# Optimization experiments

Hardware: AMD Instinct MI355X
Metric: run time of the kernel (lower is better)

Reference implementation:

```python
import jax, jax.numpy as jnp
import numpy as np

B, S, D = 2, 2048, 2048
H, KVH, DH = 16, 4, 128
WIN = 128
THETA = 10000.0  # local rope (layer_idx=0 -> local/sliding path)


def setup_inputs() -> dict:
    key = jax.random.key(0)
    ks = jax.random.split(key, 5)
    return {
        "x": jax.random.normal(ks[0], (B, S, D), dtype=jnp.float32),
        "Wq": jax.random.normal(ks[1], (H * DH, D), dtype=jnp.float32) * 0.02,
        "Wk": jax.random.normal(ks[2], (KVH * DH, D), dtype=jnp.float32) * 0.02,
        "Wv": jax.random.normal(ks[3], (KVH * DH, D), dtype=jnp.float32) * 0.02,
        "Wo": jax.random.normal(ks[4], (D, H * DH), dtype=jnp.float32) * 0.02,
    }


def _rotate_half(t):
    half = t.shape[-1] // 2
    return jnp.concatenate([-t[..., half:], t[..., :half]], axis=-1)


def _rope_tables(seq_len, head_dim, theta, dtype):
    inv_freq = 1.0 / (theta ** (jnp.arange(0, head_dim, 2, dtype=jnp.float32) / head_dim))
    freqs = jnp.arange(seq_len, dtype=jnp.float32)[:, None] * inv_freq[None, :]  # [S, DH/2]
    # source does repeat_interleave(cos, 2, dim=-1): [S, DH]
    cos = jnp.repeat(jnp.cos(freqs), 2, axis=-1).astype(dtype)
    sin = jnp.repeat(jnp.sin(freqs), 2, axis=-1).astype(dtype)
    return cos[None, :, None, :], sin[None, :, None, :]  # broadcast over [B,S,H,DH]


def reference(x, Wq, Wk, Wv, Wo):
    b, s, _ = x.shape
    q = (x @ Wq.T).reshape(b, s, H, DH)
    k = (x @ Wk.T).reshape(b, s, KVH, DH)
    v = (x @ Wv.T).reshape(b, s, KVH, DH)

    cos, sin = _rope_tables(s, DH, THETA, x.dtype)
    q = q * cos + _rotate_half(q) * sin
    k = k * cos + _rotate_half(k) * sin

    # GQA: repeat_interleave kv heads to n_heads
    groups = H // KVH
    k = jnp.repeat(k, groups, axis=2)
    v = jnp.repeat(v, groups, axis=2)

    q = q.transpose(0, 2, 1, 3)  # [B,H,S,DH]
    k = k.transpose(0, 2, 1, 3)
    v = v.transpose(0, 2, 1, 3)

    scale = DH ** -0.5
    scores = jnp.einsum('bhqd,bhkd->bhqk', q, k) * scale  # [B,H,S,S]

    # faithful local mask from source: q_idx >= k_idx - window_size
    iq = jnp.arange(s)[:, None]
    ik = jnp.arange(s)[None, :]
    mask = iq >= (ik - WIN)  # [S,S]
    scores = jnp.where(mask[None, None, :, :], scores, jnp.float32(-jnp.inf).astype(scores.dtype))

    attn = jax.nn.softmax(scores, axis=-1)
    out = jnp.einsum('bhqk,bhkd->bhqd', attn, v)
    out = out.transpose(0, 2, 1, 3).reshape(b, s, H * DH)
    return out @ Wo.T
```

## Files before the change

kernel.cpp:

```cpp
#include <hip/hip_runtime.h>
#include <hip/hip_bf16.h>

using bf16 = __hip_bfloat16;
typedef __attribute__((ext_vector_type(8))) short short8;
typedef __attribute__((ext_vector_type(4))) float floatx4;

#define AS1 __attribute__((address_space(1)))
#define AS3 __attribute__((address_space(3)))

__device__ __forceinline__ floatx4 mfma16(short8 a, short8 b, floatx4 c) {
  return __builtin_amdgcn_mfma_f32_16x16x32_bf16(a, b, c, 0, 0, 0);
}
__device__ __forceinline__ void gload16(const bf16* g, bf16* l) {
  __builtin_amdgcn_global_load_lds((const AS1 unsigned*)g, (AS3 unsigned*)l, 16, 0, 0);
}

__global__ void cast_all_k(const float* __restrict__ x, const float* __restrict__ Wq,
                           const float* __restrict__ Wk, const float* __restrict__ Wv,
                           const float* __restrict__ Wo, bf16* __restrict__ xb,
                           bf16* __restrict__ wqkv, bf16* __restrict__ wo_b) {
  int blk = blockIdx.x;
  const float* src;
  bf16* dst;
  int off;
  if (blk < 8192)       { src = x;  dst = xb;                 off = blk; }
  else if (blk < 12288) { src = Wq; dst = wqkv;               off = blk - 8192; }
  else if (blk < 13312) { src = Wk; dst = wqkv + 2048 * 2048; off = blk - 12288; }
  else if (blk < 14336) { src = Wv; dst = wqkv + 2560 * 2048; off = blk - 13312; }
  else                  { src = Wo; dst = wo_b;               off = blk - 14336; }
  int i = (off * 256 + threadIdx.x) * 4;
  float4 v = *(const float4*)(src + i);
  bf16 t[4] = {__float2bfloat16(v.x), __float2bfloat16(v.y),
               __float2bfloat16(v.z), __float2bfloat16(v.w)};
  *(ushort4*)(dst + i) = *(const ushort4*)t;
}

template <typename OutT>
__global__ __launch_bounds__(256, 2)
void gemm_bt(const bf16* __restrict__ A, const bf16* __restrict__ B,
             OutT* __restrict__ C, int M, int N, int K) {
  __shared__ alignas(16) bf16 As[128 * 32];
  __shared__ alignas(16) bf16 Bs[128 * 32];
  const int tid = threadIdx.x;
  const int w = tid >> 6, lane = tid & 63, l16 = lane & 15, quad = lane >> 4;
  const int bm = blockIdx.x << 7, bn = blockIdx.y << 7;
  const int wm = (w & 1) << 6, wn = (w >> 1) << 6;

  const int r = tid >> 2, p = tid & 3;
  const int g0 = (p ^ ((r >> 1) & 3)) << 3;
  const int g1 = (p ^ (((r + 64) >> 1) & 3)) << 3;
  const bf16* Ag0 = A + (long)(bm + r) * K + g0;
  const bf16* Ag1 = A + (long)(bm + r + 64) * K + g1;
  const bf16* Bg0 = B + (long)(bn + r) * K + g0;
  const bf16* Bg1 = B + (long)(bn + r + 64) * K + g1;
  bf16* Asw = As + (w << 9);
  bf16* Bsw = Bs + (w << 9);

  floatx4 acc[4][4];
#pragma unroll
  for (int i = 0; i < 4; ++i)
#pragma unroll
    for (int j = 0; j < 4; ++j) acc[i][j] = (floatx4)(0.0f);

  for (int k0 = 0; k0 < K; k0 += 32) {
    gload16(Ag0 + k0, Asw);
    gload16(Ag1 + k0, Asw + 2048);
    gload16(Bg0 + k0, Bsw);
    gload16(Bg1 + k0, Bsw + 2048);
    __syncthreads();
    short8 af[4], bfv[4];
#pragma unroll
    for (int mi = 0; mi < 4; ++mi) {
      int row = wm + (mi << 4) + l16;
      int pos = quad ^ ((row >> 1) & 3);
      af[mi] = *(const short8*)(As + row * 32 + pos * 8);
    }
#pragma unroll
    for (int ni = 0; ni < 4; ++ni) {
      int row = wn + (ni << 4) + l16;
      int pos = quad ^ ((row >> 1) & 3);
      bfv[ni] = *(const short8*)(Bs + row * 32 + pos * 8);
    }
#pragma unroll
    for (int mi = 0; mi < 4; ++mi)
#pragma unroll
      for (int ni = 0; ni < 4; ++ni)
        acc[mi][ni] = mfma16(af[mi], bfv[ni], acc[mi][ni]);
    __syncthreads();
  }

#pragma unroll
  for (int mi = 0; mi < 4; ++mi)
#pragma unroll
    for (int ni = 0; ni < 4; ++ni)
#pragma unroll
      for (int rr = 0; rr < 4; ++rr) {
        int row = bm + wm + (mi << 4) + (quad << 2) + rr;
        int col = bn + wn + (ni << 4) + l16;
        float v = acc[mi][ni][rr];
        if constexpr (sizeof(OutT) == 2)
          C[(long)row * N + col] = __float2bfloat16(v);
        else
          C[(long)row * N + col] = v;
      }
}

__global__ void rope_k(const bf16* __restrict__ qkv, bf16* __restrict__ Q,
                       bf16* __restrict__ Kd) {
  int idx = blockIdx.x * 256 + threadIdx.x;
  int d = idx & 63;
  int rest = idx >> 6;
  int head = rest % 20;
  int token = rest / 20;
  int s = token & 2047;
  int b = token >> 11;
  const float C0 = 0.20762050593046439f;
  float i1 = (float)(d >> 1);
  float inv1 = exp2f(-i1 * C0);
  float inv2 = exp2f(-(i1 + 32.0f) * C0);
  float a1 = (float)s * inv1, a2 = (float)s * inv2;
  float s1, c1, s2, c2;
  __sincosf(a1, &s1, &c1);
  __sincosf(a2, &s2, &c2);
  if (head < 16) {
    const bf16* p = qkv + (long)token * 3072 + head * 128 + d;
    float xlo = __bfloat162float(p[0]), xhi = __bfloat162float(p[64]);
    const float sc = 0.08838834764831845f * 1.4426950408889634f;
    float olo = (xlo * c1 - xhi * s1) * sc;
    float ohi = (xhi * c2 + xlo * s2) * sc;
    bf16* q = Q + ((long)((b << 4) + head) * 2048 + s) * 128 + d;
    q[0] = __float2bfloat16(olo);
    q[64] = __float2bfloat16(ohi);
  } else {
    int kvh = head - 16;
    const bf16* p = qkv + (long)token * 3072 + 2048 + kvh * 128 + d;
    float xlo = __bfloat162float(p[0]), xhi = __bfloat162float(p[64]);
    float olo = xlo * c1 - xhi * s1;
    float ohi = xhi * c2 + xlo * s2;
    bf16* kk = Kd + ((long)((b << 2) + kvh) * 2048 + s) * 128 + d;
    kk[0] = __float2bfloat16(olo);
    kk[64] = __float2bfloat16(ohi);
  }
}

__global__ void vtrans_k(const bf16* __restrict__ qkv, bf16* __restrict__ Vt) {
  __shared__ bf16 t[32][33];
  int x = threadIdx.x, y = threadIdx.y;
  int s0 = blockIdx.x << 5, d0 = blockIdx.y << 5, bkv = blockIdx.z;
  int b = bkv >> 2, kvh = bkv & 3;
  const bf16* src = qkv + (long)((b << 11) + s0) * 3072 + 2560 + kvh * 128 + d0;
#pragma unroll
  for (int yy = y; yy < 32; yy += 8) t[yy][x] = src[(long)yy * 3072 + x];
  __syncthreads();
  bf16* dst = Vt + (long)((bkv << 7) + d0) * 2048 + s0;
#pragma unroll
  for (int yy = y; yy < 32; yy += 8) dst[(long)yy * 2048 + x] = t[x][yy];
}

__global__ __launch_bounds__(256, 2)
void attn_k(const bf16* __restrict__ Q, const bf16* __restrict__ K,
            const bf16* __restrict__ V, bf16* __restrict__ O) {
  __shared__ alignas(16) bf16 lk[2][64 * 128];
  __shared__ alignas(16) bf16 lv[2][128 * 64];
  __shared__ alignas(16) bf16 lpA[4 * 16 * 64];
  __shared__ alignas(16) bf16 lpB[4 * 16 * 64];
  const int tid = threadIdx.x, w = tid >> 6, lane = tid & 63;
  const int l16 = lane & 15, quad = lane >> 4;
  const int bx = blockIdx.x;
  const int qa0 = bx << 6, qb0 = (31 - bx) << 6;
  const int nkA = bx + 3;
  int nkBt = 34 - bx;
  const int nkB = nkBt < 32 ? nkBt : 32;
  const int jmA = bx + 2, jmB = 33 - bx;
  const int bh = blockIdx.y, b = bh >> 4, h = bh & 15, kvh = h >> 2;
  const bf16* Qp = Q + (long)bh * 2048 * 128;
  const bf16* Kp = K + (long)((b << 2) + kvh) * 2048 * 128;
  const bf16* Vp = V + (long)((b << 2) + kvh) * 128 * 2048;

  short8 qfA[4], qfB[4];
#pragma unroll
  for (int kc = 0; kc < 4; ++kc) {
    qfA[kc] = *(const short8*)(Qp + (long)(qa0 + (w << 4) + l16) * 128 + kc * 32 + quad * 8);
    qfB[kc] = *(const short8*)(Qp + (long)(qb0 + (w << 4) + l16) * 128 + kc * 32 + quad * 8);
  }

  floatx4 oA[8], oB[8];
#pragma unroll
  for (int i = 0; i < 8; ++i) { oA[i] = (floatx4)(0.0f); oB[i] = (floatx4)(0.0f); }
  float lA = 0.0f, lB = 0.0f;

  bf16* pwA = lpA + (w << 10);
  bf16* pwB = lpB + (w << 10);
  const int sw = l16 & 7;

  auto stage = [&](int j, int bufi) {
    const int k0 = j << 6;
    bf16* lkb = &lk[bufi][0];
    bf16* lvb = &lv[bufi][0];
#pragma unroll
    for (int i = 0; i < 4; ++i) {
      int c = i * 256 + tid;
      int row = c >> 4, pos = c & 15;
      int grp = (pos & 8) | ((pos & 7) ^ (row & 7));
      gload16(Kp + (long)(k0 + row) * 128 + grp * 8, lkb + (i * 256 + (w << 6)) * 8);
    }
#pragma unroll
    for (int i = 0; i < 4; ++i) {
      int c = i * 256 + tid;
      int row = c >> 3, grp = (c & 7) ^ (row & 7);
      gload16(Vp + (long)row * 2048 + k0 + grp * 8, lvb + (i * 256 + (w << 6)) * 8);
    }
  };

  auto tile = [&](auto bothc, int k0, bool maskA, bool maskB, int bufi) {
    constexpr bool BOTH = decltype(bothc)::value;
    const bf16* lkb = &lk[bufi][0];
    const bf16* lvb = &lv[bufi][0];
    floatx4 sA[4], sB[4];
#pragma unroll
    for (int kt = 0; kt < 4; ++kt) {
      sB[kt] = (floatx4)(0.0f);
      if constexpr (BOTH) sA[kt] = (floatx4)(0.0f);
    }
#pragma unroll
    for (int kc = 0; kc < 4; ++kc) {
#pragma unroll
      for (int kt = 0; kt < 4; ++kt) {
        int row = (kt << 4) + l16;
        int g = (kc << 2) + quad;
        int pos = (g & 8) | ((g & 7) ^ (row & 7));
        short8 kf = *(const short8*)(lkb + row * 128 + pos * 8);
        sB[kt] = mfma16(kf, qfB[kc], sB[kt]);
        if constexpr (BOTH) sA[kt] = mfma16(kf, qfA[kc], sA[kt]);
      }
    }
    if (maskB) {
      int qg = qb0 + (w << 4) + l16 + 128;
#pragma unroll
      for (int kt = 0; kt < 4; ++kt)
#pragma unroll
        for (int rr = 0; rr < 4; ++rr) {
          int kg = k0 + (kt << 4) + (quad << 2) + rr;
          if (kg > qg) sB[kt][rr] = -1e30f;
        }
    }
    if constexpr (BOTH) {
      if (maskA) {
        int qg = qa0 + (w << 4) + l16 + 128;
#pragma unroll
        for (int kt = 0; kt < 4; ++kt)
#pragma unroll
          for (int rr = 0; rr < 4; ++rr) {
            int kg = k0 + (kt << 4) + (quad << 2) + rr;
            if (kg > qg) sA[kt][rr] = -1e30f;
          }
      }
    }
#pragma unroll
    for (int t = 0; t < 4; ++t) {
      int slot = (t << 2) + quad;
      int sl = ((((slot >> 1) ^ sw) << 1) | (quad & 1)) << 2;
      {
        float p0 = exp2f(sB[t][0]), p1 = exp2f(sB[t][1]);
        float p2 = exp2f(sB[t][2]), p3 = exp2f(sB[t][3]);
        lB += (p0 + p1) + (p2 + p3);
        bf16 tb[4] = {__float2bfloat16(p0), __float2bfloat16(p1),
                      __float2bfloat16(p2), __float2bfloat16(p3)};
        *(ushort4*)(pwB + (l16 << 6) + sl) = *(const ushort4*)tb;
      }
      if constexpr (BOTH) {
        float p0 = exp2f(sA[t][0]), p1 = exp2f(sA[t][1]);
        float p2 = exp2f(sA[t][2]), p3 = exp2f(sA[t][3]);
        lA += (p0 + p1) + (p2 + p3);
        bf16 ta[4] = {__float2bfloat16(p0), __float2bfloat16(p1),
                      __float2bfloat16(p2), __float2bfloat16(p3)};
        *(ushort4*)(pwA + (l16 << 6) + sl) = *(const ushort4*)ta;
      }
    }
#pragma unroll
    for (int kcl = 0; kcl < 2; ++kcl) {
      int pp = ((kcl << 2) + quad) ^ sw;
      short8 pfB = *(const short8*)(pwB + (l16 << 6) + (pp << 3));
      short8 pfA;
      if constexpr (BOTH) pfA = *(const short8*)(pwA + (l16 << 6) + (pp << 3));
      int g = (kcl << 2) + quad;
#pragma unroll
      for (int nd = 0; nd < 8; ++nd) {
        int vrow = (nd << 4) + l16;
        int vpos = g ^ (vrow & 7);
        short8 vf = *(const short8*)(lvb + vrow * 64 + (vpos << 3));
        oB[nd] = mfma16(pfB, vf, oB[nd]);
        if constexpr (BOTH) oA[nd] = mfma16(pfA, vf, oA[nd]);
      }
    }
  };

  stage(0, 0);
  __syncthreads();
  for (int j = 0; j < nkB; ++j) {
    if (j + 1 < nkB) stage(j + 1, (j + 1) & 1);
    const int k0 = j << 6;
    if (j < nkA)
      tile(std::integral_constant<bool, true>{}, k0, j == jmA, j == jmB, j & 1);
    else
      tile(std::integral_constant<bool, false>{}, k0, false, j == jmB, j & 1);
    __syncthreads();
  }

  lA += __shfl_xor(lA, 16, 64); lA += __shfl_xor(lA, 32, 64);
  lB += __shfl_xor(lB, 16, 64); lB += __shfl_xor(lB, 32, 64);
  float liA = 1.0f / lA, liB = 1.0f / lB;
  float rlA[4], rlB[4];
#pragma unroll
  for (int rr = 0; rr < 4; ++rr) {
    int src = (quad << 2) + rr;
    rlA[rr] = __shfl(liA, src, 64);
    rlB[rr] = __shfl(liB, src, 64);
  }

  bf16* OpA = O + ((long)(b << 11) + qa0 + (w << 4)) * 2048 + (h << 7);
  bf16* OpB = O + ((long)(b << 11) + qb0 + (w << 4)) * 2048 + (h << 7);
#pragma unroll
  for (int nd = 0; nd < 8; ++nd)
#pragma unroll
    for (int rr = 0; rr < 4; ++rr) {
      int row = (quad << 2) + rr;
      int col = (nd << 4) + l16;
      OpA[(long)row * 2048 + col] = __float2bfloat16(oA[nd][rr] * rlA[rr]);
      OpB[(long)row * 2048 + col] = __float2bfloat16(oB[nd][rr] * rlB[rr]);
    }
}

extern "C" void kernel_launch(void* const* d_in, const int* in_sizes, int n_in,
                              void* d_out, int out_size, void* d_ws, size_t ws_size,
                              hipStream_t stream) {
  (void)in_sizes; (void)n_in; (void)out_size; (void)ws_size;
  const float* x  = (const float*)d_in[0];
  const float* Wq = (const float*)d_in[1];
  const float* Wk = (const float*)d_in[2];
  const float* Wv = (const float*)d_in[3];
  const float* Wo = (const float*)d_in[4];
  char* ws = (char*)d_ws;
  bf16* xb   = (bf16*)(ws);
  bf16* wqkv = (bf16*)(ws + 16777216);
  bf16* wo_b = (bf16*)(ws + 29360128);
  bf16* qkv  = (bf16*)(ws + 37748736);
  bf16* Qr   = (bf16*)(ws + 62914560);
  bf16* Kr   = (bf16*)(ws + 79691776);
  bf16* Vt   = (bf16*)(ws + 83886080);
  bf16* Ob   = xb;
  float* out = (float*)d_out;

  cast_all_k<<<18432, 256, 0, stream>>>(x, Wq, Wk, Wv, Wo, xb, wqkv, wo_b);

  gemm_bt<bf16><<<dim3(32, 24), 256, 0, stream>>>(xb, wqkv, qkv, 4096, 3072, 2048);
  rope_k<<<20480, 256, 0, stream>>>(qkv, Qr, Kr);
  vtrans_k<<<dim3(64, 4, 8), dim3(32, 8), 0, stream>>>(qkv, Vt);
  attn_k<<<dim3(16, 32), 256, 0, stream>>>(Qr, Kr, Vt, Ob);
  gemm_bt<float><<<dim3(32, 16), 256, 0, stream>>>(Ob, wo_b, out, 4096, 2048, 2048);
}
```

Baseline: 294.7 us.

## Double query rows per warp in attention to reuse K/V tiles

Each attention block now handles two 128-row query tiles (paired front/back for balance) instead of two 64-row tiles, with each warp owning 32 query rows as two 16-row fragments. Every K/V fragment loaded from LDS is reused across both fragments, halving K/V global and LDS traffic per query row. In exchange the grid is halved to 256 blocks, accumulator registers double and launch bounds drop to one block per SM, lowering occupancy and latency hiding.

```diff
diff --git a/kernel.cpp b/kernel.cpp
--- a/kernel.cpp
+++ b/kernel.cpp
@@ -157,40 +157,45 @@
   for (int yy = y; yy < 32; yy += 8) dst[(long)yy * 2048 + x] = t[x][yy];
 }
 
-__global__ __launch_bounds__(256, 2)
+__global__ __launch_bounds__(256, 1)
 void attn_k(const bf16* __restrict__ Q, const bf16* __restrict__ K,
             const bf16* __restrict__ V, bf16* __restrict__ O) {
   __shared__ alignas(16) bf16 lk[2][64 * 128];
   __shared__ alignas(16) bf16 lv[2][128 * 64];
-  __shared__ alignas(16) bf16 lpA[4 * 16 * 64];
-  __shared__ alignas(16) bf16 lpB[4 * 16 * 64];
+  __shared__ alignas(16) bf16 lpA[4 * 32 * 64];
+  __shared__ alignas(16) bf16 lpB[4 * 32 * 64];
   const int tid = threadIdx.x, w = tid >> 6, lane = tid & 63;
   const int l16 = lane & 15, quad = lane >> 4;
-  const int bx = blockIdx.x;
-  const int qa0 = bx << 6, qb0 = (31 - bx) << 6;
-  const int nkA = bx + 3;
-  int nkBt = 34 - bx;
+  const int t = blockIdx.x;
+  const int qa0 = t << 7, qb0 = (15 - t) << 7;
+  const int nkA = 2 * t + 4;
+  int nkBt = 34 - 2 * t;
   const int nkB = nkBt < 32 ? nkBt : 32;
-  const int jmA = bx + 2, jmB = 33 - bx;
+  const int jmA0 = 2 * t + 2, jmB0 = 32 - 2 * t;
   const int bh = blockIdx.y, b = bh >> 4, h = bh & 15, kvh = h >> 2;
   const bf16* Qp = Q + (long)bh * 2048 * 128;
   const bf16* Kp = K + (long)((b << 2) + kvh) * 2048 * 128;
   const bf16* Vp = V + (long)((b << 2) + kvh) * 128 * 2048;
-
-  short8 qfA[4], qfB[4];
-#pragma unroll
-  for (int kc = 0; kc < 4; ++kc) {
-    qfA[kc] = *(const short8*)(Qp + (long)(qa0 + (w << 4) + l16) * 128 + kc * 32 + quad * 8);
-    qfB[kc] = *(const short8*)(Qp + (long)(qb0 + (w << 4) + l16) * 128 + kc * 32 + quad * 8);
-  }
-
-  floatx4 oA[8], oB[8];
-#pragma unroll
-  for (int i = 0; i < 8; ++i) { oA[i] = (floatx4)(0.0f); oB[i] = (floatx4)(0.0f); }
-  float lA = 0.0f, lB = 0.0f;
-
-  bf16* pwA = lpA + (w << 10);
-  bf16* pwB = lpB + (w << 10);
+  const int wq = w << 5;
+
+  short8 qfA[2][4], qfB[2][4];
+#pragma unroll
+  for (int f = 0; f < 2; ++f)
+#pragma unroll
+    for (int kc = 0; kc < 4; ++kc) {
+      qfA[f][kc] = *(const short8*)(Qp + (long)(qa0 + wq + (f << 4) + l16) * 128 + kc * 32 + quad * 8);
+      qfB[f][kc] = *(const short8*)(Qp + (long)(qb0 + wq + (f << 4) + l16) * 128 + kc * 32 + quad * 8);
+    }
+
+  floatx4 oA[8][2], oB[8][2];
+#pragma unroll
+  for (int i = 0; i < 8; ++i)
+#pragma unroll
+    for (int f = 0; f < 2; ++f) { oA[i][f] = (floatx4)(0.0f); oB[i][f] = (floatx4)(0.0f); }
+  float lA[2] = {0.0f, 0.0f}, lB[2] = {0.0f, 0.0f};
+
+  bf16* pwA = lpA + (w << 11);
+  bf16* pwB = lpB + (w << 11);
   const int sw = l16 & 7;
 
   auto stage = [&](int j, int bufi) {
@@ -216,12 +221,14 @@
     constexpr bool BOTH = decltype(bothc)::value;
     const bf16* lkb = &lk[bufi][0];
     const bf16* lvb = &lv[bufi][0];
-    floatx4 sA[4], sB[4];
-#pragma unroll
-    for (int kt = 0; kt < 4; ++kt) {
-      sB[kt] = (floatx4)(0.0f);
-      if constexpr (BOTH) sA[kt] = (floatx4)(0.0f);
-    }
+    floatx4 sA[4][2], sB[4][2];
+#pragma unroll
+    for (int kt = 0; kt < 4; ++kt)
+#pragma unroll
+      for (int f = 0; f < 2; ++f) {
+        sB[kt][f] = (floatx4)(0.0f);
+        if constexpr (BOTH) sA[kt][f] = (floatx4)(0.0f);
+      }
 #pragma unroll
     for (int kc = 0; kc < 4; ++kc) {
 #pragma unroll
@@ -230,67 +237,86 @@
         int g = (kc << 2) + quad;
         int pos = (g & 8) | ((g & 7) ^ (row & 7));
         short8 kf = *(const short8*)(lkb + row * 128 + pos * 8);
-        sB[kt] = mfma16(kf, qfB[kc], sB[kt]);
-        if constexpr (BOTH) sA[kt] = mfma16(kf, qfA[kc], sA[kt]);
+#pragma unroll
+        for (int f = 0; f < 2; ++f) {
+          sB[kt][f] = mfma16(kf, qfB[f][kc], sB[kt][f]);
+          if constexpr (BOTH) sA[kt][f] = mfma16(kf, qfA[f][kc], sA[kt][f]);
+        }
       }
     }
     if (maskB) {
-      int qg = qb0 + (w << 4) + l16 + 128;
-#pragma unroll
-      for (int kt = 0; kt < 4; ++kt)
-#pragma unroll
-        for (int rr = 0; rr < 4; ++rr) {
-          int kg = k0 + (kt << 4) + (quad << 2) + rr;
-          if (kg > qg) sB[kt][rr] = -1e30f;
-        }
+#pragma unroll
+      for (int f = 0; f < 2; ++f) {
+        int qg = qb0 + wq + (f << 4) + l16 + 128;
+#pragma unroll
+        for (int kt = 0; kt < 4; ++kt)
+#pragma unroll
+          for (int rr = 0; rr < 4; ++rr) {
+            int kg = k0 + (kt << 4) + (quad << 2) + rr;
+            if (kg > qg) sB[kt][f][rr] = -1e30f;
+          }
+      }
     }
     if constexpr (BOTH) {
       if (maskA) {
-        int qg = qa0 + (w << 4) + l16 + 128;
-#pragma unroll
-        for (int kt = 0; kt < 4; ++kt)
-#pragma unroll
-          for (int rr = 0; rr < 4; ++rr) {
-            int kg = k0 + (kt << 4) + (quad << 2) + rr;
-            if (kg > qg) sA[kt][rr] = -1e30f;
-          }
-      }
-    }
-#pragma unroll
-    for (int t = 0; t < 4; ++t) {
-      int slot = (t << 2) + quad;
-      int sl = ((((slot >> 1) ^ sw) << 1) | (quad & 1)) << 2;
-      {
-        float p0 = exp2f(sB[t][0]), p1 = exp2f(sB[t][1]);
-        float p2 = exp2f(sB[t][2]), p3 = exp2f(sB[t][3]);
-        lB += (p0 + p1) + (p2 + p3);
-        bf16 tb[4] = {__float2bfloat16(p0), __float2bfloat16(p1),
-                      __float2bfloat16(p2), __float2bfloat16(p3)};
-        *(ushort4*)(pwB + (l16 << 6) + sl) = *(const ushort4*)tb;
-      }
-      if constexpr (BOTH) {
-        float p0 = exp2f(sA[t][0]), p1 = exp2f(sA[t][1]);
-        float p2 = exp2f(sA[t][2]), p3 = exp2f(sA[t][3]);
-        lA += (p0 + p1) + (p2 + p3);
-        bf16 ta[4] = {__float2bfloat16(p0), __float2bfloat16(p1),
-                      __float2bfloat16(p2), __float2bfloat16(p3)};
-        *(ushort4*)(pwA + (l16 << 6) + sl) = *(const ushort4*)ta;
+#pragma unroll
+        for (int f = 0; f < 2; ++f) {
+          int qg = qa0 + wq + (f << 4) + l16 + 128;
+#pragma unroll
+          for (int kt = 0; kt < 4; ++kt)
+#pragma unroll
+            for (int rr = 0; rr < 4; ++rr) {
+              int kg = k0 + (kt << 4) + (quad << 2) + rr;
+              if (kg > qg) sA[kt][f][rr] = -1e30f;
+            }
+        }
+      }
+    }
+#pragma unroll
+    for (int f = 0; f < 2; ++f) {
+      int qrow = ((f << 4) + l16) << 6;
+#pragma unroll
+      for (int kt = 0; kt < 4; ++kt) {
+        int g = (kt << 1) + (quad >> 1);
+        int sl = (((g ^ sw) << 1) | (quad & 1)) << 2;
+        {
+          float p0 = exp2f(sB[kt][f][0]), p1 = exp2f(sB[kt][f][1]);
+          float p2 = exp2f(sB[kt][f][2]), p3 = exp2f(sB[kt][f][3]);
+          lB[f] += (p0 + p1) + (p2 + p3);
+          bf16 tb[4] = {__float2bfloat16(p0), __float2bfloat16(p1),
+                        __float2bfloat16(p2), __float2bfloat16(p3)};
+          *(ushort4*)(pwB + qrow + sl) = *(const ushort4*)tb;
+        }
+        if constexpr (BOTH) {
+          float p0 = exp2f(sA[kt][f][0]), p1 = exp2f(sA[kt][f][1]);
+          float p2 = exp2f(sA[kt][f][2]), p3 = exp2f(sA[kt][f][3]);
+          lA[f] += (p0 + p1) + (p2 + p3);
+          bf16 ta[4] = {__float2bfloat16(p0), __float2bfloat16(p1),
+                        __float2bfloat16(p2), __float2bfloat16(p3)};
+          *(ushort4*)(pwA + qrow + sl) = *(const ushort4*)ta;
+        }
       }
     }
 #pragma unroll
     for (int kcl = 0; kcl < 2; ++kcl) {
-      int pp = ((kcl << 2) + quad) ^ sw;
-      short8 pfB = *(const short8*)(pwB + (l16 << 6) + (pp << 3));
-      short8 pfA;
-      if constexpr (BOTH) pfA = *(const short8*)(pwA + (l16 << 6) + (pp << 3));
+      int pp = (((kcl << 2) + quad) ^ sw) << 3;
+      short8 pfB[2], pfA[2];
+#pragma unroll
+      for (int f = 0; f < 2; ++f) {
+        pfB[f] = *(const short8*)(pwB + (((f << 4) + l16) << 6) + pp);
+        if constexpr (BOTH) pfA[f] = *(const short8*)(pwA + (((f << 4) + l16) << 6) + pp);
+      }
       int g = (kcl << 2) + quad;
 #pragma unroll
       for (int nd = 0; nd < 8; ++nd) {
         int vrow = (nd << 4) + l16;
         int vpos = g ^ (vrow & 7);
         short8 vf = *(const short8*)(lvb + vrow * 64 + (vpos << 3));
-        oB[nd] = mfma16(pfB, vf, oB[nd]);
-        if constexpr (BOTH) oA[nd] = mfma16(pfA, vf, oA[nd]);
+#pragma unroll
+        for (int f = 0; f < 2; ++f) {
+          oB[nd][f] = mfma16(pfB[f], vf, oB[nd][f]);
+          if constexpr (BOTH) oA[nd][f] = mfma16(pfA[f], vf, oA[nd][f]);
+        }
       }
     }
   };
@@ -300,35 +326,45 @@
   for (int j = 0; j < nkB; ++j) {
     if (j + 1 < nkB) stage(j + 1, (j + 1) & 1);
     const int k0 = j << 6;
+    bool mA = (j == jmA0) | (j == jmA0 + 1);
+    bool mB = (j == jmB0) | (j == jmB0 + 1);
     if (j < nkA)
-      tile(std::integral_constant<bool, true>{}, k0, j == jmA, j == jmB, j & 1);
+      tile(std::integral_constant<bool, true>{}, k0, mA, mB, j & 1);
     else
-      tile(std::integral_constant<bool, false>{}, k0, false, j == jmB, j & 1);
+      tile(std::integral_constant<bool, false>{}, k0, false, mB, j & 1);
     __syncthreads();
   }
 
-  lA += __shfl_xor(lA, 16, 64); lA += __shfl_xor(lA, 32, 64);
-  lB += __shfl_xor(lB, 16, 64); lB += __shfl_xor(lB, 32, 64);
-  float liA = 1.0f / lA, liB = 1.0f / lB;
-  float rlA[4], rlB[4];
-#pragma unroll
-  for (int rr = 0; rr < 4; ++rr) {
-    int src = (quad << 2) + rr;
-    rlA[rr] = __shfl(liA, src, 64);
-    rlB[rr] = __shfl(liB, src, 64);
-  }
-
-  bf16* OpA = O + ((long)(b << 11) + qa0 + (w << 4)) * 2048 + (h << 7);
-  bf16* OpB = O + ((long)(b << 11) + qb0 + (w << 4)) * 2048 + (h << 7);
-#pragma unroll
-  for (int nd = 0; nd < 8; ++nd)
+#pragma unroll
+  for (int f = 0; f < 2; ++f) {
+    lA[f] += __shfl_xor(lA[f], 16, 64); lA[f] += __shfl_xor(lA[f], 32, 64);
+    lB[f] += __shfl_xor(lB[f], 16, 64); lB[f] += __shfl_xor(lB[f], 32, 64);
+  }
+  float rlA[2][4], rlB[2][4];
+#pragma unroll
+  for (int f = 0; f < 2; ++f) {
+    float liA = 1.0f / lA[f], liB = 1.0f / lB[f];
 #pragma unroll
     for (int rr = 0; rr < 4; ++rr) {
-      int row = (quad << 2) + rr;
-      int col = (nd << 4) + l16;
-      OpA[(long)row * 2048 + col] = __float2bfloat16(oA[nd][rr] * rlA[rr]);
-      OpB[(long)row * 2048 + col] = __float2bfloat16(oB[nd][rr] * rlB[rr]);
-    }
+      int src = (quad << 2) + rr;
+      rlA[f][rr] = __shfl(liA, src, 64);
+      rlB[f][rr] = __shfl(liB, src, 64);
+    }
+  }
+
+  bf16* OpA = O + ((long)(b << 11) + qa0 + wq) * 2048 + (h << 7);
+  bf16* OpB = O + ((long)(b << 11) + qb0 + wq) * 2048 + (h << 7);
+#pragma unroll
+  for (int f = 0; f < 2; ++f)
+#pragma unroll
+    for (int nd = 0; nd < 8; ++nd)
+#pragma unroll
+      for (int rr = 0; rr < 4; ++rr) {
+        int row = (f << 4) + (quad << 2) + rr;
+        int col = (nd << 4) + l16;
+        OpA[(long)row * 2048 + col] = __float2bfloat16(oA[nd][f][rr] * rlA[f][rr]);
+        OpB[(long)row * 2048 + col] = __float2bfloat16(oB[nd][f][rr] * rlB[f][rr]);
+      }
 }
 
 extern "C" void kernel_launch(void* const* d_in, const int* in_sizes, int n_in,
@@ -356,6 +392,6 @@
   gemm_bt<bf16><<<dim3(32, 24), 256, 0, stream>>>(xb, wqkv, qkv, 4096, 3072, 2048);
   rope_k<<<20480, 256, 0, stream>>>(qkv, Qr, Kr);
   vtrans_k<<<dim3(64, 4, 8), dim3(32, 8), 0, stream>>>(qkv, Vt);
-  attn_k<<<dim3(16, 32), 256, 0, stream>>>(Qr, Kr, Vt, Ob);
+  attn_k<<<dim3(8, 32), 256, 0, stream>>>(Qr, Kr, Vt, Ob);
   gemm_bt<float><<<dim3(32, 16), 256, 0, stream>>>(Ob, wo_b, out, 4096, 2048, 2048);
 }
```

Result: slower. 324.4 us (+10.1%).

## Rewrite local attention with 32x32x16 MFMA, register P shuffle, and adjacent q-block pairing

Applied to the files above, without the earlier changes.

Moves the attention kernel from 16x16x32 MFMA tiles to 32x32x16 tiles, so each wave covers 32 query rows (16 rows from each of two adjacent 64-row blocks). The softmax probabilities are repacked into MFMA operand layout with cross-half wave shuffles, which removes the LDS round-trip for P. Work is also reassigned: each block now takes an adjacent pair of q-blocks, and the order is reversed for the second batch to balance load. The aim is fewer LDS accesses and fewer MFMA issues, at the cost of more shuffles and register pressure. The grid dimension in the launch code must now match the new mapping.

```diff
diff --git a/kernel.cpp b/kernel.cpp
--- a/kernel.cpp
+++ b/kernel.cpp
@@ -4,6 +4,7 @@
 using bf16 = __hip_bfloat16;
 typedef __attribute__((ext_vector_type(8))) short short8;
 typedef __attribute__((ext_vector_type(4))) float floatx4;
+typedef __attribute__((ext_vector_type(16))) float floatx16;
 
 #define AS1 __attribute__((address_space(1)))
 #define AS3 __attribute__((address_space(3)))
@@ -11,8 +12,15 @@
 __device__ __forceinline__ floatx4 mfma16(short8 a, short8 b, floatx4 c) {
   return __builtin_amdgcn_mfma_f32_16x16x32_bf16(a, b, c, 0, 0, 0);
 }
+__device__ __forceinline__ floatx16 mfma32(short8 a, short8 b, floatx16 c) {
+  return __builtin_amdgcn_mfma_f32_32x32x16_bf16(a, b, c, 0, 0, 0);
+}
 __device__ __forceinline__ void gload16(const bf16* g, bf16* l) {
   __builtin_amdgcn_global_load_lds((const AS1 unsigned*)g, (AS3 unsigned*)l, 16, 0, 0);
+}
+__device__ __forceinline__ unsigned short f2b(float x) {
+  bf16 t = __float2bfloat16(x);
+  return *reinterpret_cast<unsigned short*>(&t);
 }
 
 __global__ void cast_all_k(const float* __restrict__ x, const float* __restrict__ Wq,
@@ -162,36 +170,30 @@
             const bf16* __restrict__ V, bf16* __restrict__ O) {
   __shared__ alignas(16) bf16 lk[2][64 * 128];
   __shared__ alignas(16) bf16 lv[2][128 * 64];
-  __shared__ alignas(16) bf16 lpA[4 * 16 * 64];
-  __shared__ alignas(16) bf16 lpB[4 * 16 * 64];
   const int tid = threadIdx.x, w = tid >> 6, lane = tid & 63;
-  const int l16 = lane & 15, quad = lane >> 4;
-  const int bx = blockIdx.x;
-  const int qa0 = bx << 6, qb0 = (31 - bx) << 6;
-  const int nkA = bx + 3;
-  int nkBt = 34 - bx;
-  const int nkB = nkBt < 32 ? nkBt : 32;
-  const int jmA = bx + 2, jmB = 33 - bx;
-  const int bh = blockIdx.y, b = bh >> 4, h = bh & 15, kvh = h >> 2;
+  const int cl = lane & 31, h = lane >> 5;
+  const int bh = blockIdx.y, b = bh >> 4, hh = bh & 15, kvh = hh >> 2;
+  const int t = (bh < 16) ? blockIdx.x : (15 - blockIdx.x);
+  const int qa0 = (2 * t) << 6, qb0 = (2 * t + 1) << 6;
+  int nkt = 2 * t + 4;
+  const int nkB = nkt < 32 ? nkt : 32;
+  const int jmA = 2 * t + 2, jmB = 2 * t + 3;
   const bf16* Qp = Q + (long)bh * 2048 * 128;
   const bf16* Kp = K + (long)((b << 2) + kvh) * 2048 * 128;
   const bf16* Vp = V + (long)((b << 2) + kvh) * 128 * 2048;
-
-  short8 qfA[4], qfB[4];
-#pragma unroll
-  for (int kc = 0; kc < 4; ++kc) {
-    qfA[kc] = *(const short8*)(Qp + (long)(qa0 + (w << 4) + l16) * 128 + kc * 32 + quad * 8);
-    qfB[kc] = *(const short8*)(Qp + (long)(qb0 + (w << 4) + l16) * 128 + kc * 32 + quad * 8);
-  }
-
-  floatx4 oA[8], oB[8];
-#pragma unroll
-  for (int i = 0; i < 8; ++i) { oA[i] = (floatx4)(0.0f); oB[i] = (floatx4)(0.0f); }
-  float lA = 0.0f, lB = 0.0f;
-
-  bf16* pwA = lpA + (w << 10);
-  bf16* pwB = lpB + (w << 10);
-  const int sw = l16 & 7;
+  const int wq = w << 4;
+  const int qpos = (cl < 16) ? (qa0 + wq + cl) : (qb0 + wq + (cl - 16));
+  const int jm_lane = (cl < 16) ? jmA : jmB;
+
+  short8 qf[8];
+#pragma unroll
+  for (int ks = 0; ks < 8; ++ks)
+    qf[ks] = *(const short8*)(Qp + (long)qpos * 128 + ks * 16 + h * 8);
+
+  floatx16 o[4];
+#pragma unroll
+  for (int dt = 0; dt < 4; ++dt) o[dt] = (floatx16)(0.0f);
+  float lsum = 0.0f;
 
   auto stage = [&](int j, int bufi) {
     const int k0 = j << 6;
@@ -212,123 +214,97 @@
     }
   };
 
-  auto tile = [&](auto bothc, int k0, bool maskA, bool maskB, int bufi) {
-    constexpr bool BOTH = decltype(bothc)::value;
-    const bf16* lkb = &lk[bufi][0];
-    const bf16* lvb = &lv[bufi][0];
-    floatx4 sA[4], sB[4];
-#pragma unroll
-    for (int kt = 0; kt < 4; ++kt) {
-      sB[kt] = (floatx4)(0.0f);
-      if constexpr (BOTH) sA[kt] = (floatx4)(0.0f);
-    }
-#pragma unroll
-    for (int kc = 0; kc < 4; ++kc) {
-#pragma unroll
-      for (int kt = 0; kt < 4; ++kt) {
-        int row = (kt << 4) + l16;
-        int g = (kc << 2) + quad;
-        int pos = (g & 8) | ((g & 7) ^ (row & 7));
-        short8 kf = *(const short8*)(lkb + row * 128 + pos * 8);
-        sB[kt] = mfma16(kf, qfB[kc], sB[kt]);
-        if constexpr (BOTH) sA[kt] = mfma16(kf, qfA[kc], sA[kt]);
-      }
-    }
-    if (maskB) {
-      int qg = qb0 + (w << 4) + l16 + 128;
-#pragma unroll
-      for (int kt = 0; kt < 4; ++kt)
-#pragma unroll
-        for (int rr = 0; rr < 4; ++rr) {
-          int kg = k0 + (kt << 4) + (quad << 2) + rr;
-          if (kg > qg) sB[kt][rr] = -1e30f;
-        }
-    }
-    if constexpr (BOTH) {
-      if (maskA) {
-        int qg = qa0 + (w << 4) + l16 + 128;
-#pragma unroll
-        for (int kt = 0; kt < 4; ++kt)
-#pragma unroll
-          for (int rr = 0; rr < 4; ++rr) {
-            int kg = k0 + (kt << 4) + (quad << 2) + rr;
-            if (kg > qg) sA[kt][rr] = -1e30f;
-          }
-      }
-    }
-#pragma unroll
-    for (int t = 0; t < 4; ++t) {
-      int slot = (t << 2) + quad;
-      int sl = ((((slot >> 1) ^ sw) << 1) | (quad & 1)) << 2;
-      {
-        float p0 = exp2f(sB[t][0]), p1 = exp2f(sB[t][1]);
-        float p2 = exp2f(sB[t][2]), p3 = exp2f(sB[t][3]);
-        lB += (p0 + p1) + (p2 + p3);
-        bf16 tb[4] = {__float2bfloat16(p0), __float2bfloat16(p1),
-                      __float2bfloat16(p2), __float2bfloat16(p3)};
-        *(ushort4*)(pwB + (l16 << 6) + sl) = *(const ushort4*)tb;
-      }
-      if constexpr (BOTH) {
-        float p0 = exp2f(sA[t][0]), p1 = exp2f(sA[t][1]);
-        float p2 = exp2f(sA[t][2]), p3 = exp2f(sA[t][3]);
-        lA += (p0 + p1) + (p2 + p3);
-        bf16 ta[4] = {__float2bfloat16(p0), __float2bfloat16(p1),
-                      __float2bfloat16(p2), __float2bfloat16(p3)};
-        *(ushort4*)(pwA + (l16 << 6) + sl) = *(const ushort4*)ta;
-      }
-    }
-#pragma unroll
-    for (int kcl = 0; kcl < 2; ++kcl) {
-      int pp = ((kcl << 2) + quad) ^ sw;
-      short8 pfB = *(const short8*)(pwB + (l16 << 6) + (pp << 3));
-      short8 pfA;
-      if constexpr (BOTH) pfA = *(const short8*)(pwA + (l16 << 6) + (pp << 3));
-      int g = (kcl << 2) + quad;
-#pragma unroll
-      for (int nd = 0; nd < 8; ++nd) {
-        int vrow = (nd << 4) + l16;
-        int vpos = g ^ (vrow & 7);
-        short8 vf = *(const short8*)(lvb + vrow * 64 + (vpos << 3));
-        oB[nd] = mfma16(pfB, vf, oB[nd]);
-        if constexpr (BOTH) oA[nd] = mfma16(pfA, vf, oA[nd]);
-      }
-    }
-  };
-
   stage(0, 0);
   __syncthreads();
   for (int j = 0; j < nkB; ++j) {
     if (j + 1 < nkB) stage(j + 1, (j + 1) & 1);
     const int k0 = j << 6;
-    if (j < nkA)
-      tile(std::integral_constant<bool, true>{}, k0, j == jmA, j == jmB, j & 1);
-    else
-      tile(std::integral_constant<bool, false>{}, k0, false, j == jmB, j & 1);
+    const bf16* lkb = &lk[j & 1][0];
+    const bf16* lvb = &lv[j & 1][0];
+
+    floatx16 s[2];
+    s[0] = (floatx16)(0.0f);
+    s[1] = (floatx16)(0.0f);
+#pragma unroll
+    for (int ks = 0; ks < 8; ++ks) {
+      int g = 2 * ks + h;
+#pragma unroll
+      for (int kt = 0; kt < 2; ++kt) {
+        int row = (kt << 5) + cl;
+        int pos = (g & 8) | ((g & 7) ^ (row & 7));
+        short8 kf = *(const short8*)(lkb + row * 128 + pos * 8);
+        s[kt] = mfma32(kf, qf[ks], s[kt]);
+      }
+    }
+
+    if (j >= jmA) {
+      int qlim = (j < jm_lane) ? 0x7fffffff : ((j == jm_lane) ? (qpos + 128) : -1);
+#pragma unroll
+      for (int kt = 0; kt < 2; ++kt)
+#pragma unroll
+        for (int r = 0; r < 16; ++r) {
+          int key = k0 + (kt << 5) + (r & 3) + ((r >> 2) << 3) + (h << 2);
+          if (key > qlim) s[kt][r] = -1e30f;
+        }
+    }
+
+#pragma unroll
+    for (int kt = 0; kt < 2; ++kt)
+#pragma unroll
+      for (int r = 0; r < 16; ++r) {
+        float p = exp2f(s[kt][r]);
+        lsum += p;
+        s[kt][r] = p;
+      }
+
+#pragma unroll
+    for (int kt = 0; kt < 2; ++kt) {
+#pragma unroll
+      for (int kk = 0; kk < 2; ++kk) {
+        float sd0 = h ? s[kt][8 * kk + 0] : s[kt][8 * kk + 4];
+        float sd1 = h ? s[kt][8 * kk + 1] : s[kt][8 * kk + 5];
+        float sd2 = h ? s[kt][8 * kk + 2] : s[kt][8 * kk + 6];
+        float sd3 = h ? s[kt][8 * kk + 3] : s[kt][8 * kk + 7];
+        float rc0 = __shfl_xor(sd0, 32);
+        float rc1 = __shfl_xor(sd1, 32);
+        float rc2 = __shfl_xor(sd2, 32);
+        float rc3 = __shfl_xor(sd3, 32);
+        float lo0 = h ? rc0 : s[kt][8 * kk + 0];
+        float lo1 = h ? rc1 : s[kt][8 * kk + 1];
+        float lo2 = h ? rc2 : s[kt][8 * kk + 2];
+        float lo3 = h ? rc3 : s[kt][8 * kk + 3];
+        float hi0 = h ? s[kt][8 * kk + 4] : rc0;
+        float hi1 = h ? s[kt][8 * kk + 5] : rc1;
+        float hi2 = h ? s[kt][8 * kk + 6] : rc2;
+        float hi3 = h ? s[kt][8 * kk + 7] : rc3;
+        union { short8 v; unsigned short u[8]; } pf;
+        pf.u[0] = f2b(lo0); pf.u[1] = f2b(lo1); pf.u[2] = f2b(lo2); pf.u[3] = f2b(lo3);
+        pf.u[4] = f2b(hi0); pf.u[5] = f2b(hi1); pf.u[6] = f2b(hi2); pf.u[7] = f2b(hi3);
+        int g = (kt << 2) + (kk << 1) + h;
+#pragma unroll
+        for (int dt = 0; dt < 4; ++dt) {
+          int vrow = (dt << 5) + cl;
+          int vpos = g ^ (vrow & 7);
+          short8 vf = *(const short8*)(lvb + vrow * 64 + (vpos << 3));
+          o[dt] = mfma32(pf.v, vf, o[dt]);
+        }
+      }
+    }
     __syncthreads();
   }
 
-  lA += __shfl_xor(lA, 16, 64); lA += __shfl_xor(lA, 32, 64);
-  lB += __shfl_xor(lB, 16, 64); lB += __shfl_xor(lB, 32, 64);
-  float liA = 1.0f / lA, liB = 1.0f / lB;
-  float rlA[4], rlB[4];
-#pragma unroll
-  for (int rr = 0; rr < 4; ++rr) {
-    int src = (quad << 2) + rr;
-    rlA[rr] = __shfl(liA, src, 64);
-    rlB[rr] = __shfl(liB, src, 64);
+  lsum += __shfl_xor(lsum, 32);
+  float li = 1.0f / lsum;
+  bf16* Ob = O + ((long)(b << 11)) * 2048 + (hh << 7) + cl;
+#pragma unroll
+  for (int r = 0; r < 16; ++r) {
+    int m = (r & 3) + ((r >> 2) << 3) + (h << 2);
+    float rl = __shfl(li, m);
+    long row = (m < 16) ? (qa0 + wq + m) : (qb0 + wq + (m - 16));
+#pragma unroll
+    for (int dt = 0; dt < 4; ++dt)
+      Ob[row * 2048 + dt * 32] = __float2bfloat16(o[dt][r] * rl);
   }
-
-  bf16* OpA = O + ((long)(b << 11) + qa0 + (w << 4)) * 2048 + (h << 7);
-  bf16* OpB = O + ((long)(b << 11) + qb0 + (w << 4)) * 2048 + (h << 7);
-#pragma unroll
-  for (int nd = 0; nd < 8; ++nd)
-#pragma unroll
-    for (int rr = 0; rr < 4; ++rr) {
-      int row = (quad << 2) + rr;
-      int col = (nd << 4) + l16;
-      OpA[(long)row * 2048 + col] = __float2bfloat16(oA[nd][rr] * rlA[rr]);
-      OpB[(long)row * 2048 + col] = __float2bfloat16(oB[nd][rr] * rlB[rr]);
-    }
 }
 
 extern "C" void kernel_launch(void* const* d_in, const int* in_sizes, int n_in,
```

After: 302.4 us. +2.6%, slower.
